# Kernel optimization log

Hardware: AMD Instinct MI355X
Metric: run time of the kernel (lower is better)

## Reference

```python
import jax, jax.numpy as jnp
import numpy as np

NUM_NODES = 50000
NUM_OBSERVED = 512
BATCH = 2048


def setup_inputs() -> dict:
    key = jax.random.key(0)
    inputs = jax.random.normal(key, (BATCH, NUM_OBSERVED), dtype=jnp.float32)
    # 512 unique, strided node ids in [0, NUM_NODES): 511*97 = 49567 < 50000
    node_indices = (jnp.arange(NUM_OBSERVED, dtype=jnp.int64) * 97)
    return {"inputs": inputs, "node_indices": node_indices}


def reference(inputs, node_indices):
    # Faithful to: full = inputs @ one_hot(node_indices, NUM_NODES); full[..., None]
    # One-hot matmul sums contributions at duplicate indices, so scatter-ADD
    # (not set) reproduces the exact math without the dense [K, N] GEMM.
    batch = inputs.shape[0]
    full = jnp.zeros((batch, NUM_NODES), dtype=inputs.dtype)
    full = full.at[:, node_indices].add(inputs)  # [B, N]
    return full[..., None]  # [B, N, 1]
```

## Files before the change

kernel.cpp:

```cpp
#include <hip/hip_runtime.h>


#define TPB 256
#define BLOCKS 2048

typedef float v4f __attribute__((ext_vector_type(4)));

__global__ void pmap_init_kernel(int* __restrict__ pmap, int n4) {
    int i = blockIdx.x * blockDim.x + threadIdx.x;
    if (i < n4) pmap[i] = -1;
}

__global__ void pmap_fill_kernel(const int* __restrict__ idx, int k,
                                 int* __restrict__ pmap) {
    int j = blockIdx.x * blockDim.x + threadIdx.x;
    if (j < k) {
        int n = idx[j];
        pmap[n >> 2] = (j << 2) | (n & 3);
    }
}

__global__ __launch_bounds__(TPB) void fused_flat_kernel(
    const float* __restrict__ in,
    const int*   __restrict__ pmap,
    float*       __restrict__ out,
    int K, int n4, unsigned total4)
{
    const unsigned stride = gridDim.x * TPB;
    unsigned g = blockIdx.x * TPB + threadIdx.x;
    if (g >= total4) return;

    unsigned b = g / (unsigned)n4;
    unsigned c = g - b * (unsigned)n4;
    const unsigned sdiv = stride / (unsigned)n4;
    const unsigned smod = stride - sdiv * (unsigned)n4;

    v4f* out4 = (v4f*)out;

    for (; g < total4; g += stride) {
        const int pm = pmap[c];
        v4f v = (v4f)(0.f);
        if (pm >= 0) {
            const float val = in[(size_t)b * K + (pm >> 2)];
            const int slot = pm & 3;
            if (slot == 0) v.x = val;
            else if (slot == 1) v.y = val;
            else if (slot == 2) v.z = val;
            else v.w = val;
        }
        __builtin_nontemporal_store(v, out4 + g);

        b += sdiv; c += smod;
        if (c >= (unsigned)n4) { c -= (unsigned)n4; ++b; }
    }
}

extern "C" void kernel_launch(void* const* d_in, const int* in_sizes, int n_in,
                              void* d_out, int out_size, void* d_ws, size_t ws_size,
                              hipStream_t stream) {
    const float* in  = (const float*)d_in[0];
    const int*   idx = (const int*)d_in[1];
    float*       out = (float*)d_out;

    const int K = in_sizes[1];
    const int B = in_sizes[0] / K;
    const int N = out_size / B;
    const int n4 = N / 4;
    const unsigned total4 = (unsigned)B * (unsigned)n4;

    int* pmap = (int*)d_ws;

    pmap_init_kernel<<<(n4 + 255) / 256, 256, 0, stream>>>(pmap, n4);
    pmap_fill_kernel<<<(K + 255) / 256, 256, 0, stream>>>(idx, K, pmap);

    fused_flat_kernel<<<BLOCKS, TPB, 0, stream>>>(in, pmap, out, K, n4, total4);
}
```

Measured before the change: 434.7 us.

## Replace grid-stride flat kernel with 2D banded kernel reusing pmap across rows

Swaps the persistent grid-stride loop over the flat output for a 2D grid, where each thread owns one float4 column group and writes 8 batch rows. The pmap entry is loaded once per thread and reused across those rows. Input loads are issued unconditionally, with index 0 standing in for empty columns, and the one-hot vector is built without branches. This removes the per-iteration div/mod bookkeeping and divergent branches, but launches many more blocks and adds redundant input reads for empty columns. It also assumes B is divisible by 8.

Result: faster. 406.1 us (-6.6%).

```diff
diff --git a/kernel.cpp b/kernel.cpp
--- a/kernel.cpp
+++ b/kernel.cpp
@@ -2,7 +2,7 @@
 
 
 #define TPB 256
-#define BLOCKS 2048
+#define ROWS 8
 
 typedef float v4f __attribute__((ext_vector_type(4)));
 
@@ -20,39 +20,39 @@
     }
 }
 
-__global__ __launch_bounds__(TPB) void fused_flat_kernel(
+__device__ __forceinline__ v4f make_group(int pm, float val) {
+    v4f v;
+    const int slot = pm & 3;
+    v.x = (pm >= 0 && slot == 0) ? val : 0.f;
+    v.y = (pm >= 0 && slot == 1) ? val : 0.f;
+    v.z = (pm >= 0 && slot == 2) ? val : 0.f;
+    v.w = (pm >= 0 && slot == 3) ? val : 0.f;
+    return v;
+}
+
+__global__ __launch_bounds__(TPB) void banded_branchless_kernel(
     const float* __restrict__ in,
     const int*   __restrict__ pmap,
     float*       __restrict__ out,
-    int K, int n4, unsigned total4)
+    int K, int n4)
 {
-    const unsigned stride = gridDim.x * TPB;
-    unsigned g = blockIdx.x * TPB + threadIdx.x;
-    if (g >= total4) return;
+    const int g = blockIdx.x * TPB + threadIdx.x;
+    if (g >= n4) return;
+    const int b0 = blockIdx.y * ROWS;
 
-    unsigned b = g / (unsigned)n4;
-    unsigned c = g - b * (unsigned)n4;
-    const unsigned sdiv = stride / (unsigned)n4;
-    const unsigned smod = stride - sdiv * (unsigned)n4;
+    const int pm = pmap[g];
+    const int j  = (pm < 0) ? 0 : (pm >> 2);
 
-    v4f* out4 = (v4f*)out;
+    const float* col = in + (size_t)b0 * K + j;
+    v4f* p = (v4f*)out + (size_t)b0 * n4 + g;
 
-    for (; g < total4; g += stride) {
-        const int pm = pmap[c];
-        v4f v = (v4f)(0.f);
-        if (pm >= 0) {
-            const float val = in[(size_t)b * K + (pm >> 2)];
-            const int slot = pm & 3;
-            if (slot == 0) v.x = val;
-            else if (slot == 1) v.y = val;
-            else if (slot == 2) v.z = val;
-            else v.w = val;
-        }
-        __builtin_nontemporal_store(v, out4 + g);
-
-        b += sdiv; c += smod;
-        if (c >= (unsigned)n4) { c -= (unsigned)n4; ++b; }
-    }
+    float val[ROWS];
+#pragma unroll
+    for (int r = 0; r < ROWS; ++r)
+        val[r] = col[(size_t)r * K];
+#pragma unroll
+    for (int r = 0; r < ROWS; ++r)
+        __builtin_nontemporal_store(make_group(pm, val[r]), p + (size_t)r * n4);
 }
 
 extern "C" void kernel_launch(void* const* d_in, const int* in_sizes, int n_in,
@@ -66,12 +66,12 @@
     const int B = in_sizes[0] / K;
     const int N = out_size / B;
     const int n4 = N / 4;
-    const unsigned total4 = (unsigned)B * (unsigned)n4;
 
     int* pmap = (int*)d_ws;
 
     pmap_init_kernel<<<(n4 + 255) / 256, 256, 0, stream>>>(pmap, n4);
     pmap_fill_kernel<<<(K + 255) / 256, 256, 0, stream>>>(idx, K, pmap);
 
-    fused_flat_kernel<<<BLOCKS, TPB, 0, stream>>>(in, pmap, out, K, n4, total4);
+    dim3 grid((n4 + TPB - 1) / TPB, B / ROWS);
+    banded_branchless_kernel<<<grid, TPB, 0, stream>>>(in, pmap, out, K, n4);
 }
```
